# Kernel optimization log

Hardware: AMD Instinct MI355X
Metric: run time of the kernel (lower is better)

Reference implementation:

```python
import jax, jax.numpy as jnp
from jax import lax
import numpy as np

# StyleLayer config (see init_kwargs)
B, CIN, COUT, SDIM, K, H, W = 8, 512, 512, 512, 3, 64, 64
UP, DOWN = 2, 2
PAD = (9, 8, 9, 8)            # px0, px1, py0, py1 (computed in __init__)
GAIN = 2.0 ** 0.5             # non-rgb gain
SLOPE = 0.2                   # non-rgb negative slope
CLAMP = 256.0                 # conv_clamp
TAPS = 12                     # filter_size * factor
TMP_SRATE = 128.0             # max(sr_in, sr_out) * lrelu_sampling
CUTOFF = 32.0
WIDTH = 32.0                  # half_width * 2


def _kaiser_lowpass(numtaps, cutoff, width, fs):
    """Equivalent of scipy.signal.firwin(numtaps, cutoff, width=width, fs=fs)."""
    nyq = fs / 2.0
    atten = 2.285 * (numtaps - 1) * np.pi * (width / nyq) + 7.95  # kaiser_atten
    if atten > 50:
        beta = 0.1102 * (atten - 8.7)
    elif atten > 21:
        beta = 0.5842 * (atten - 21) ** 0.4 + 0.07886 * (atten - 21)
    else:
        beta = 0.0
    m = np.arange(numtaps) - (numtaps - 1) / 2.0
    fc = cutoff / nyq
    h = fc * np.sinc(fc * m) * np.kaiser(numtaps, beta)
    h /= h.sum()
    return jnp.asarray(h, jnp.float32)


def _upfirdn2d_sep(x, f, up, down, padding, gain):
    """upfirdn2d reference with separable 1D filter (flip_filter=False)."""
    Bx, C, Hx, Wx = x.shape
    px0, px1, py0, py1 = padding
    if up > 1:  # zero insertion
        x = x.reshape(Bx, C, Hx, 1, Wx, 1)
        x = jnp.pad(x, [(0, 0), (0, 0), (0, 0), (0, up - 1), (0, 0), (0, up - 1)])
        x = x.reshape(Bx, C, Hx * up, Wx * up)
    x = jnp.pad(x, [(0, 0), (0, 0), (py0, py1), (px0, px1)])
    fk = (f * (gain ** 0.5))[::-1].astype(x.dtype)  # gain**(ndim/2) per pass, flipped
    t = fk.shape[0]
    dn = ('NCHW', 'OIHW', 'NCHW')
    kx = jnp.tile(fk.reshape(1, 1, 1, t), (C, 1, 1, 1))
    x = lax.conv_general_dilated(x, kx, (1, 1), [(0, 0), (0, 0)], dimension_numbers=dn, feature_group_count=C)
    ky = jnp.tile(fk.reshape(1, 1, t, 1), (C, 1, 1, 1))
    x = lax.conv_general_dilated(x, ky, (1, 1), [(0, 0), (0, 0)], dimension_numbers=dn, feature_group_count=C)
    if down > 1:
        x = x[:, :, ::down, ::down]
    return x


def setup_inputs() -> dict:
    key = jax.random.key(0)
    ks = jax.random.split(key, 4)
    f = _kaiser_lowpass(TAPS, CUTOFF, WIDTH, TMP_SRATE)
    return {
        'x': jax.random.normal(ks[0], (B, CIN, H, W), jnp.float32),
        'w': jax.random.normal(ks[1], (B, SDIM), jnp.float32),
        'affine_weight': jax.random.normal(ks[2], (CIN, SDIM), jnp.float32),
        'affine_bias': jnp.ones((CIN,), jnp.float32),  # bias.data.fill_(1.0)
        'conv_weight': jax.random.normal(ks[3], (COUT, CIN, K, K), jnp.float32),
        'bias': jnp.zeros((COUT,), jnp.float32),
        'up_filter': f,
        'down_filter': f,
        'ema': jnp.ones((1,), jnp.float32),
    }


def reference(x, w, affine_weight, affine_bias, conv_weight, bias, up_filter, down_filter, ema):
    input_gain = lax.rsqrt(ema[0])
    # affine: Linear with scale = 1/sqrt(style_dim), linear activation
    s = w @ (affine_weight * (1.0 / SDIM ** 0.5)).T + affine_bias            # [B, CIN]
    # modulated conv weight construction
    wt = conv_weight[None] * s[:, None, :, None, None] * (1.0 / (CIN * K * K) ** 0.5)
    d = lax.rsqrt(jnp.sum(jnp.square(wt), axis=(2, 3, 4)) + 1e-8)            # demod
    wt = wt * d[:, :, None, None, None] * input_gain
    # grouped conv: one group per sample, padding = kernel_size - 1
    xg = x.reshape(1, B * CIN, H, W)
    wg = wt.reshape(B * COUT, CIN, K, K)
    y = lax.conv_general_dilated(xg, wg, (1, 1), [(K - 1, K - 1), (K - 1, K - 1)],
                                 dimension_numbers=('NCHW', 'OIHW', 'NCHW'),
                                 feature_group_count=B)
    y = y.reshape(B, COUT, H + K - 1, W + K - 1)
    # filtered_lrelu reference: bias -> up-FIR (gain=up^2) -> lrelu*gain, clamp -> FIR-down
    y = y + bias[None, :, None, None]
    y = _upfirdn2d_sep(y, up_filter, UP, 1, PAD, float(UP * UP))
    y = jnp.clip(jnp.where(y >= 0, y, y * SLOPE) * GAIN, -CLAMP, CLAMP)
    y = _upfirdn2d_sep(y, down_filter, 1, DOWN, (0, 0, 0, 0), 1.0)
    return y
```

## Files before the change

### kernel.cpp

```cpp
#include <hip/hip_runtime.h>
#include <hip/hip_bf16.h>


#define B_    8
#define CIN_  512
#define COUT_ 512
#define SDIM_ 512
#define H_    64
#define W_    64
#define HO_   66
#define NPIX  4356
#define XP    68

typedef short s8v  __attribute__((ext_vector_type(8)));
typedef float f4v  __attribute__((ext_vector_type(4)));

#define WAITV3() asm volatile("s_waitcnt vmcnt(3)" ::: "memory")
#define WAITV0() asm volatile("s_waitcnt vmcnt(0)" ::: "memory")

__global__ __launch_bounds__(256) void k_style_s(
    const float* __restrict__ w, const float* __restrict__ aw,
    const float* __restrict__ ab, float* __restrict__ s) {
    const int t  = blockIdx.x * 4 + (threadIdx.x >> 6);
    const int ln = threadIdx.x & 63;
    const int b = t >> 9, c = t & 511;
    const float* wp = w + b * SDIM_;
    const float* ap = aw + (size_t)c * SDIM_;
    float acc = 0.f;
    #pragma unroll
    for (int j = 0; j < 8; ++j) { int k = ln + 64 * j; acc += wp[k] * ap[k]; }
    #pragma unroll
    for (int off = 32; off; off >>= 1) acc += __shfl_down(acc, off, 64);
    if (ln == 0) s[t] = acc * 0.044194173824159216f + ab[c];
}

__global__ __launch_bounds__(256) void k_style_coef(
    const float* __restrict__ s, const float* __restrict__ r,
    const float* __restrict__ ema, float* __restrict__ coef) {
    const int t  = blockIdx.x * 4 + (threadIdx.x >> 6);
    const int ln = threadIdx.x & 63;
    const int b = t >> 9, o = t & 511;
    const float* sp = s + b * 512;
    const float* rp = r + (size_t)o * 512;
    float acc = 0.f;
    #pragma unroll
    for (int j = 0; j < 8; ++j) {
        int k = ln + 64 * j;
        float sv = sp[k];
        acc += sv * sv * rp[k];
    }
    #pragma unroll
    for (int off = 32; off; off >>= 1) acc += __shfl_down(acc, off, 64);
    if (ln == 0) {
        float d  = rsqrtf(acc * (1.0f / 4608.0f) + 1e-8f);
        coef[t] = d * rsqrtf(ema[0]) * 0.014731391274719739f;
    }
}

__global__ __launch_bounds__(256) void k_prep_w(const float* __restrict__ cw,
                                                __hip_bfloat16* __restrict__ wb,
                                                float* __restrict__ r) {
    __shared__ float sm[2304];
    const int base = blockIdx.x * 256;
    const int tid  = threadIdx.x;
    const float* src = cw + (size_t)base * 9;
    for (int i = tid; i < 2304; i += 256) sm[i] = src[i];
    __syncthreads();
    float a = 0.f;
    ushort u[9];
    #pragma unroll
    for (int k = 0; k < 9; ++k) {
        float v = sm[tid * 9 + k];
        a += v * v;
        __hip_bfloat16 h = __float2bfloat16(v);
        u[k] = *reinterpret_cast<ushort*>(&h);
    }
    r[base + tid] = a;
    ushort* wbu = reinterpret_cast<ushort*>(wb);
    #pragma unroll
    for (int tap = 0; tap < 9; ++tap)
        wbu[tap * 262144 + base + tid] = u[tap];
}

__global__ __launch_bounds__(256) void k_prep_x(const float* __restrict__ x,
                                                const float* __restrict__ s,
                                                __hip_bfloat16* __restrict__ xt) {
    __shared__ float tile[64][65];
    const int y = blockIdx.x;
    const int b = blockIdx.y;
    const int tid = threadIdx.x;
    const bool yin = (y >= 2 && y < 66);
    __hip_bfloat16* orow = xt + ((size_t)(b * XP + y)) * XP * 512;
    for (int c0 = 0; c0 < 512; c0 += 64) {
        if (yin) {
            for (int i = tid; i < 64 * 64; i += 256) {
                int c = i >> 6, xx = i & 63;
                tile[c][xx] = x[(((size_t)b * 512 + c0 + c) * 64 + (y - 2)) * 64 + xx]
                              * s[b * 512 + c0 + c];
            }
        }
        __syncthreads();
        for (int j = tid; j < 68 * 8; j += 256) {
            int xx = j >> 3, cg = j & 7;
            bool xin = yin && (xx >= 2 && xx < 66);
            union { ushort u[8]; float4 f4; } pk;
            #pragma unroll
            for (int k = 0; k < 8; ++k) {
                float v = xin ? tile[cg * 8 + k][xx - 2] : 0.f;
                __hip_bfloat16 h = __float2bfloat16(v);
                pk.u[k] = *reinterpret_cast<ushort*>(&h);
            }
            *reinterpret_cast<float4*>(orow + (size_t)xx * 512 + c0 + cg * 8) = pk.f4;
        }
        __syncthreads();
    }
}

__device__ __forceinline__ void gload16u(const char* base, unsigned voff, void* l) {
    __builtin_amdgcn_global_load_lds(
        (const __attribute__((address_space(1))) unsigned*)(base + voff),
        (__attribute__((address_space(3))) unsigned*)l, 16, 0, 0);
}

__global__ __launch_bounds__(512) void k_conv_mfma(
    const __hip_bfloat16* __restrict__ wb, const __hip_bfloat16* __restrict__ xt,
    const float* __restrict__ coef, const float* __restrict__ bias,
    __hip_bfloat16* __restrict__ y1)
{
    __shared__ __hip_bfloat16 lds[3][12288];

    const int bid   = blockIdx.x;
    const int dbl   = bid < 48;
    const int rr2   = dbl ? bid : bid - 48;
    const int xcd   = rr2 & 7;
    const int j     = dbl ? (rr2 >> 3) : (6 + (rr2 >> 3));
    const int ntile = dbl ? 2 : 1;

    const int tid = threadIdx.x, wv = tid >> 6, ln = tid & 63;
    const int wm = wv >> 1, wn = wv & 1;

    const int srow = tid >> 2, ssl = tid & 3;
    const unsigned swzs = (unsigned)((ssl ^ ((srow >> 1) & 3)) << 3);
    int aoff[4], boff[4];
    #pragma unroll
    for (int f = 0; f < 4; ++f) {
        int r  = wm * 64 + f * 16 + (ln & 15);
        aoff[f] = (r * 32 + (((ln >> 4) ^ ((r >> 1) & 3)) << 3)) * 2;
        int rb = wn * 64 + f * 16 + (ln & 15);
        boff[f] = (8192 + rb * 32 + (((ln >> 4) ^ ((rb >> 1) & 3)) << 3)) * 2;
    }
    const char* wbB = (const char*)wb;

    for (int tt = 0; tt < ntile; ++tt) {
        const int pos  = (tt == 0) ? j : (64 + j);
        const int flat = xcd * 70 + pos;
        const int pi = flat % 35;
        const int t2 = flat / 35;
        const int b  = t2 & 7;
        const int o0 = (t2 >> 3) * 256;
        const int p0 = pi * 128;

        const char* xtB = (const char*)(xt + (size_t)b * XP * XP * 512);
        unsigned voffA0 = ((unsigned)(o0 + srow) * 512u + swzs) * 2u;
        unsigned voffA1 = ((unsigned)(o0 + 128 + srow) * 512u + swzs) * 2u;
        unsigned voffB0;
        {
            int p = p0 + srow; if (p > NPIX - 1) p = NPIX - 1;
            int py = (int)(((unsigned)p * 63551u) >> 22);
            int px = p - py * 66;
            voffB0 = ((unsigned)(py * XP + px) * 512u + swzs) * 2u;
        }

        f4v acc[4][4];
        #pragma unroll
        for (int fm = 0; fm < 4; ++fm)
            #pragma unroll
            for (int fn = 0; fn < 4; ++fn) acc[fm][fn] = (f4v){0.f, 0.f, 0.f, 0.f};

        auto stage = [&](int st, int buf) {
            int tap = st >> 4;
            int ki  = (tap * 11) >> 5;
            int kj  = tap - ki * 3;
            unsigned ccb  = (unsigned)(st & 15) << 6;
            unsigned offA = (unsigned)tap * 524288u + ccb;
            unsigned offB = (unsigned)(ki * XP + kj) * 1024u + ccb;
            __hip_bfloat16* dst = &lds[buf][0] + wv * 512;
            gload16u(wbB, voffA0 + offA, dst);
            gload16u(wbB, voffA1 + offA, dst + 4096);
            gload16u(xtB, voffB0 + offB, dst + 8192);
        };

        auto compute = [&](int buf) {
            const char* base = (const char*)&lds[buf][0];
            s8v af[4], bfv[4];
            #pragma unroll
            for (int f = 0; f < 4; ++f) {
                af[f]  = *reinterpret_cast<const s8v*>(base + aoff[f]);
                bfv[f] = *reinterpret_cast<const s8v*>(base + boff[f]);
            }
            #pragma unroll
            for (int fm = 0; fm < 4; ++fm)
                #pragma unroll
                for (int fn = 0; fn < 4; ++fn)
                    acc[fm][fn] = __builtin_amdgcn_mfma_f32_16x16x32_bf16(
                        af[fm], bfv[fn], acc[fm][fn], 0, 0, 0);
        };

        stage(0, 0);
        stage(1, 1);

        #pragma unroll 1
        for (int st = 0; st < 141; st += 3) {
            WAITV3(); __builtin_amdgcn_s_barrier();
            compute(0); stage(st + 2, 2);
            WAITV3(); __builtin_amdgcn_s_barrier();
            compute(1); stage(st + 3, 0);
            WAITV3(); __builtin_amdgcn_s_barrier();
            compute(2); stage(st + 4, 1);
        }
        WAITV3(); __builtin_amdgcn_s_barrier();
        compute(0); stage(143, 2);
        WAITV3(); __builtin_amdgcn_s_barrier();
        compute(1);
        WAITV0(); __builtin_amdgcn_s_barrier();
        compute(2);

        #pragma unroll
        for (int fm = 0; fm < 4; ++fm) {
            #pragma unroll
            for (int fn = 0; fn < 4; ++fn) {
                int p = p0 + wn * 64 + fn * 16 + (ln & 15);
                if (p < NPIX) {
                    int ob = o0 + wm * 64 + fm * 16 + (ln >> 4) * 4;
                    #pragma unroll
                    for (int jj = 0; jj < 4; ++jj) {
                        int o = ob + jj;
                        float v = acc[fm][fn][jj] * coef[b * 512 + o] + bias[o];
                        y1[((size_t)(b * 512 + o)) * NPIX + p] = __float2bfloat16(v);
                    }
                }
            }
        }
    }
}

__global__ __launch_bounds__(256) void k_style_fir(
    const __hip_bfloat16* __restrict__ y1, const float* __restrict__ uf,
    const float* __restrict__ df, float* __restrict__ out)
{
    __shared__ float smA[5632];
    __shared__ float smB[3200];
    float* It = smA;
    float* hu = smB;
    float* zt = smA;
    float* dh = smB;

    const int img = blockIdx.z;
    const int oy0 = blockIdx.y * 32;
    const int ox0 = blockIdx.x * 32;
    const int tid = threadIdx.x;
    const __hip_bfloat16* I = y1 + (size_t)img * NPIX;

    float cu[12], cd[12];
    #pragma unroll
    for (int q = 0; q < 12; ++q) { cu[q] = uf[q]; cd[q] = df[q]; }

    const int ty = tid >> 5, tx = tid & 31;
    const int ty4 = tid >> 4, tx4 = tid & 15;

    #pragma unroll
    for (int k = 0; k < 6; ++k) {
        int rr = ty + 8 * k; if (rr >= 42) break;
        int gy = oy0 - 4 + rr;
        bool yin = (gy >= 0 && gy < HO_);
        #pragma unroll
        for (int j = 0; j < 2; ++j) {
            int cc = tx + 32 * j; if (cc >= 42) continue;
            int gx = ox0 - 4 + cc;
            float v = 0.f;
            if (yin && gx >= 0 && gx < HO_) v = __bfloat162float(I[gy * HO_ + gx]);
            It[rr * 44 + cc] = v;
        }
    }
    __syncthreads();

    #pragma unroll
    for (int k = 0; k < 6; ++k) {
        int m = ty + 8 * k; if (m >= 42) break;
        #pragma unroll
        for (int j = 0; j < 2; ++j) {
            int h = tx + 32 * j; if (h >= 37) continue;
            float v[6];
            #pragma unroll
            for (int q = 0; q < 6; ++q) v[q] = It[m * 44 + h + 5 - q];
            float e = 0.f, o = 0.f;
            #pragma unroll
            for (int q = 0; q < 6; ++q) { e += cu[2 * q] * v[q]; o += cu[2 * q + 1] * v[q]; }
            *reinterpret_cast<float2*>(hu + m * 76 + 2 * h) = make_float2(2.f * e, 2.f * o);
        }
    }
    __syncthreads();

    {
        int rx  = tid % 74;
        int seg = tid / 74;
        if (seg < 3) {
            int r0  = seg * 13;
            int cnt = (seg == 2) ? 11 : 13;
            float wnd[6];
            #pragma unroll
            for (int i = 0; i < 5; ++i) wnd[i] = hu[(r0 + i) * 76 + rx];
            #pragma unroll
            for (int i = 0; i < 13; ++i) {
                if (i < cnt) {
                    wnd[5] = hu[(r0 + i + 5) * 76 + rx];
                    float e = 0.f, o = 0.f;
                    #pragma unroll
                    for (int q = 0; q < 6; ++q) {
                        e += cu[2 * q] * wnd[5 - q];
                        o += cu[2 * q + 1] * wnd[5 - q];
                    }
                    e *= 2.f; o *= 2.f;
                    e = (e >= 0.f ? e : e * 0.2f) * 1.4142135623730951f;
                    o = (o >= 0.f ? o : o * 0.2f) * 1.4142135623730951f;
                    e = fminf(fmaxf(e, -256.f), 256.f);
                    o = fminf(fmaxf(o, -256.f), 256.f);
                    int r = r0 + i;
                    zt[(2 * r) * 76 + rx]     = e;
                    zt[(2 * r + 1) * 76 + rx] = o;
                    #pragma unroll
                    for (int k2 = 0; k2 < 5; ++k2) wnd[k2] = wnd[k2 + 1];
                }
            }
        }
    }
    __syncthreads();

    #pragma unroll
    for (int k = 0; k < 5; ++k) {
        int ry = ty4 + 16 * k; if (ry >= 74) break;
        const float* zr = zt + ry * 76 + 4 * tx4;
        float z[14];
        #pragma unroll
        for (int t = 0; t < 7; ++t) {
            float2 p2 = *reinterpret_cast<const float2*>(zr + 2 * t);
            z[2 * t] = p2.x; z[2 * t + 1] = p2.y;
        }
        float a0 = 0.f, a1 = 0.f;
        #pragma unroll
        for (int u = 0; u < 12; ++u) { a0 += z[u] * cd[11 - u]; a1 += z[u + 2] * cd[11 - u]; }
        *reinterpret_cast<float2*>(dh + ry * 36 + 2 * tx4) = make_float2(a0, a1);
    }
    __syncthreads();

    #pragma unroll
    for (int k = 0; k < 2; ++k) {
        int r2 = ty + 8 * k;
        float d[14];
        #pragma unroll
        for (int v = 0; v < 14; ++v) d[v] = dh[(4 * r2 + v) * 36 + tx];
        float a0 = 0.f, a1 = 0.f;
        #pragma unroll
        for (int v = 0; v < 12; ++v) { a0 += d[v] * cd[11 - v]; a1 += d[v + 2] * cd[11 - v]; }
        float* op = out + (size_t)img * 64 * 64 + (oy0 + 2 * r2) * 64 + ox0 + tx;
        op[0]  = a0;
        op[64] = a1;
    }
}

extern "C" void kernel_launch(void* const* d_in, const int* in_sizes, int n_in,
                              void* d_out, int out_size, void* d_ws, size_t ws_size,
                              hipStream_t stream) {
    const float* x    = (const float*)d_in[0];
    const float* w    = (const float*)d_in[1];
    const float* aw   = (const float*)d_in[2];
    const float* ab   = (const float*)d_in[3];
    const float* cw   = (const float*)d_in[4];
    const float* bias = (const float*)d_in[5];
    const float* uf   = (const float*)d_in[6];
    const float* df   = (const float*)d_in[7];
    const float* ema  = (const float*)d_in[8];
    float* out = (float*)d_out;

    float* ws   = (float*)d_ws;
    float* s_   = ws;
    float* coef = ws + 4096;
    float* r_   = ws + 8192;
    __hip_bfloat16* y1 = (__hip_bfloat16*)(ws + 270336);
    __hip_bfloat16* xt = (__hip_bfloat16*)(ws + 270336 + 8921088);
    __hip_bfloat16* wb = (__hip_bfloat16*)(ws + 270336 + 8921088 + 9469952);

    k_style_s   <<<1024, 256, 0, stream>>>(w, aw, ab, s_);
    k_prep_w    <<<1024, 256, 0, stream>>>(cw, wb, r_);
    k_style_coef<<<1024, 256, 0, stream>>>(s_, r_, ema, coef);
    k_prep_x    <<<dim3(68, 8), 256, 0, stream>>>(x, s_, xt);
    k_conv_mfma <<<512, 512, 0, stream>>>(wb, xt, coef, bias, y1);
    k_style_fir <<<dim3(2, 2, 4096), 256, 0, stream>>>(y1, uf, df, out);
}
```

Measured before the change: 361.3 us.

## Widen conv pixel tile to 160 and drop the double-tile block scheduling

Changes the implicit-GEMM conv tile from 256x128 to 256x160 output pixels, giving 448 blocks that each handle exactly one tile instead of the previous mix of one- and two-tile blocks. The last tile overlaps the previous one to avoid bounds checks, and two extra waves load the additional B rows with an adjusted vmcnt wait. The aim is better load balance across the 256 CUs and more MFMA work per staged A tile, at the cost of more accumulator registers, larger LDS buffers, and some redundant computation in the overlapping tile.

```diff
diff --git a/kernel.cpp b/kernel.cpp
--- a/kernel.cpp
+++ b/kernel.cpp
@@ -15,6 +15,7 @@
 typedef short s8v  __attribute__((ext_vector_type(8)));
 typedef float f4v  __attribute__((ext_vector_type(4)));
 
+#define WAITV4() asm volatile("s_waitcnt vmcnt(4)" ::: "memory")
 #define WAITV3() asm volatile("s_waitcnt vmcnt(3)" ::: "memory")
 #define WAITV0() asm volatile("s_waitcnt vmcnt(0)" ::: "memory")
 
@@ -122,123 +123,131 @@
         (__attribute__((address_space(3))) unsigned*)l, 16, 0, 0);
 }
 
-__global__ __launch_bounds__(512) void k_conv_mfma(
+__global__ __launch_bounds__(512, 4) void k_conv_mfma(
     const __hip_bfloat16* __restrict__ wb, const __hip_bfloat16* __restrict__ xt,
     const float* __restrict__ coef, const float* __restrict__ bias,
     __hip_bfloat16* __restrict__ y1)
 {
-    __shared__ __hip_bfloat16 lds[3][12288];
-
-    const int bid   = blockIdx.x;
-    const int dbl   = bid < 48;
-    const int rr2   = dbl ? bid : bid - 48;
-    const int xcd   = rr2 & 7;
-    const int j     = dbl ? (rr2 >> 3) : (6 + (rr2 >> 3));
-    const int ntile = dbl ? 2 : 1;
+    __shared__ __hip_bfloat16 lds[3][13312];
+
+    const int bid  = blockIdx.x;
+    const int flat = (bid & 7) * 56 + (bid >> 3);
+    const int pi = flat % 28;
+    const int t2 = flat / 28;
+    const int b  = t2 & 7;
+    const int o0 = (t2 >> 3) * 256;
+    const int p0 = (pi < 27) ? pi * 160 : (NPIX - 160);
 
     const int tid = threadIdx.x, wv = tid >> 6, ln = tid & 63;
     const int wm = wv >> 1, wn = wv & 1;
 
+    const char* wbB = (const char*)wb;
+    const char* xtB = (const char*)(xt + (size_t)b * XP * XP * 512);
     const int srow = tid >> 2, ssl = tid & 3;
     const unsigned swzs = (unsigned)((ssl ^ ((srow >> 1) & 3)) << 3);
-    int aoff[4], boff[4];
+    unsigned voffA0 = ((unsigned)(o0 + srow) * 512u + swzs) * 2u;
+    unsigned voffA1 = ((unsigned)(o0 + 128 + srow) * 512u + swzs) * 2u;
+    unsigned voffB0, voffB1 = 0;
+    {
+        int p = p0 + srow;
+        int py = (int)(((unsigned)p * 63551u) >> 22);
+        int px = p - py * 66;
+        voffB0 = ((unsigned)(py * XP + px) * 512u + swzs) * 2u;
+    }
+    if (wv < 2) {
+        int j2 = 512 + tid;
+        int row2 = j2 >> 2, sl2 = j2 & 3;
+        unsigned swz2 = (unsigned)((sl2 ^ ((row2 >> 1) & 3)) << 3);
+        int p = p0 + row2;
+        int py = (int)(((unsigned)p * 63551u) >> 22);
+        int px = p - py * 66;
+        voffB1 = ((unsigned)(py * XP + px) * 512u + swz2) * 2u;
+    }
+
+    int aoff[4], boff[5];
     #pragma unroll
     for (int f = 0; f < 4; ++f) {
         int r  = wm * 64 + f * 16 + (ln & 15);
         aoff[f] = (r * 32 + (((ln >> 4) ^ ((r >> 1) & 3)) << 3)) * 2;
-        int rb = wn * 64 + f * 16 + (ln & 15);
+    }
+    #pragma unroll
+    for (int f = 0; f < 5; ++f) {
+        int rb = wn * 80 + f * 16 + (ln & 15);
         boff[f] = (8192 + rb * 32 + (((ln >> 4) ^ ((rb >> 1) & 3)) << 3)) * 2;
     }
-    const char* wbB = (const char*)wb;
-
-    for (int tt = 0; tt < ntile; ++tt) {
-        const int pos  = (tt == 0) ? j : (64 + j);
-        const int flat = xcd * 70 + pos;
-        const int pi = flat % 35;
-        const int t2 = flat / 35;
-        const int b  = t2 & 7;
-        const int o0 = (t2 >> 3) * 256;
-        const int p0 = pi * 128;
-
-        const char* xtB = (const char*)(xt + (size_t)b * XP * XP * 512);
-        unsigned voffA0 = ((unsigned)(o0 + srow) * 512u + swzs) * 2u;
-        unsigned voffA1 = ((unsigned)(o0 + 128 + srow) * 512u + swzs) * 2u;
-        unsigned voffB0;
-        {
-            int p = p0 + srow; if (p > NPIX - 1) p = NPIX - 1;
-            int py = (int)(((unsigned)p * 63551u) >> 22);
-            int px = p - py * 66;
-            voffB0 = ((unsigned)(py * XP + px) * 512u + swzs) * 2u;
-        }
-
-        f4v acc[4][4];
-        #pragma unroll
-        for (int fm = 0; fm < 4; ++fm)
-            #pragma unroll
-            for (int fn = 0; fn < 4; ++fn) acc[fm][fn] = (f4v){0.f, 0.f, 0.f, 0.f};
-
-        auto stage = [&](int st, int buf) {
-            int tap = st >> 4;
-            int ki  = (tap * 11) >> 5;
-            int kj  = tap - ki * 3;
-            unsigned ccb  = (unsigned)(st & 15) << 6;
-            unsigned offA = (unsigned)tap * 524288u + ccb;
-            unsigned offB = (unsigned)(ki * XP + kj) * 1024u + ccb;
-            __hip_bfloat16* dst = &lds[buf][0] + wv * 512;
-            gload16u(wbB, voffA0 + offA, dst);
-            gload16u(wbB, voffA1 + offA, dst + 4096);
-            gload16u(xtB, voffB0 + offB, dst + 8192);
-        };
-
-        auto compute = [&](int buf) {
-            const char* base = (const char*)&lds[buf][0];
-            s8v af[4], bfv[4];
-            #pragma unroll
-            for (int f = 0; f < 4; ++f) {
-                af[f]  = *reinterpret_cast<const s8v*>(base + aoff[f]);
-                bfv[f] = *reinterpret_cast<const s8v*>(base + boff[f]);
-            }
+
+    f4v acc[4][5];
+    #pragma unroll
+    for (int fm = 0; fm < 4; ++fm)
+        #pragma unroll
+        for (int fn = 0; fn < 5; ++fn) acc[fm][fn] = (f4v){0.f, 0.f, 0.f, 0.f};
+
+    auto stage = [&](int st, int buf) {
+        int tap = st >> 4;
+        int ki  = (tap * 11) >> 5;
+        int kj  = tap - ki * 3;
+        unsigned ccb  = (unsigned)(st & 15) << 6;
+        unsigned offA = (unsigned)tap * 524288u + ccb;
+        unsigned offB = (unsigned)(ki * XP + kj) * 1024u + ccb;
+        __hip_bfloat16* dst = &lds[buf][0] + wv * 512;
+        gload16u(wbB, voffA0 + offA, dst);
+        gload16u(wbB, voffA1 + offA, dst + 4096);
+        gload16u(xtB, voffB0 + offB, dst + 8192);
+        if (wv < 2)
+            gload16u(xtB, voffB1 + offB, dst + 12288);
+    };
+
+    auto compute = [&](int buf) {
+        const char* base = (const char*)&lds[buf][0];
+        s8v af[4];
+        #pragma unroll
+        for (int f = 0; f < 4; ++f)
+            af[f] = *reinterpret_cast<const s8v*>(base + aoff[f]);
+        #pragma unroll
+        for (int fn = 0; fn < 5; ++fn) {
+            s8v bv = *reinterpret_cast<const s8v*>(base + boff[fn]);
             #pragma unroll
             for (int fm = 0; fm < 4; ++fm)
-                #pragma unroll
-                for (int fn = 0; fn < 4; ++fn)
-                    acc[fm][fn] = __builtin_amdgcn_mfma_f32_16x16x32_bf16(
-                        af[fm], bfv[fn], acc[fm][fn], 0, 0, 0);
-        };
-
-        stage(0, 0);
-        stage(1, 1);
-
-        #pragma unroll 1
-        for (int st = 0; st < 141; st += 3) {
-            WAITV3(); __builtin_amdgcn_s_barrier();
-            compute(0); stage(st + 2, 2);
-            WAITV3(); __builtin_amdgcn_s_barrier();
-            compute(1); stage(st + 3, 0);
-            WAITV3(); __builtin_amdgcn_s_barrier();
-            compute(2); stage(st + 4, 1);
-        }
-        WAITV3(); __builtin_amdgcn_s_barrier();
-        compute(0); stage(143, 2);
-        WAITV3(); __builtin_amdgcn_s_barrier();
-        compute(1);
-        WAITV0(); __builtin_amdgcn_s_barrier();
-        compute(2);
-
-        #pragma unroll
-        for (int fm = 0; fm < 4; ++fm) {
-            #pragma unroll
-            for (int fn = 0; fn < 4; ++fn) {
-                int p = p0 + wn * 64 + fn * 16 + (ln & 15);
-                if (p < NPIX) {
-                    int ob = o0 + wm * 64 + fm * 16 + (ln >> 4) * 4;
-                    #pragma unroll
-                    for (int jj = 0; jj < 4; ++jj) {
-                        int o = ob + jj;
-                        float v = acc[fm][fn][jj] * coef[b * 512 + o] + bias[o];
-                        y1[((size_t)(b * 512 + o)) * NPIX + p] = __float2bfloat16(v);
-                    }
-                }
+                acc[fm][fn] = __builtin_amdgcn_mfma_f32_16x16x32_bf16(
+                    af[fm], bv, acc[fm][fn], 0, 0, 0);
+        }
+    };
+
+    stage(0, 0);
+    stage(1, 1);
+
+    #pragma unroll 1
+    for (int st = 0; st < 141; st += 3) {
+        if (wv < 2) { WAITV4(); } else { WAITV3(); }
+        __builtin_amdgcn_s_barrier();
+        compute(0); stage(st + 2, 2);
+        if (wv < 2) { WAITV4(); } else { WAITV3(); }
+        __builtin_amdgcn_s_barrier();
+        compute(1); stage(st + 3, 0);
+        if (wv < 2) { WAITV4(); } else { WAITV3(); }
+        __builtin_amdgcn_s_barrier();
+        compute(2); stage(st + 4, 1);
+    }
+    if (wv < 2) { WAITV4(); } else { WAITV3(); }
+    __builtin_amdgcn_s_barrier();
+    compute(0); stage(143, 2);
+    if (wv < 2) { WAITV4(); } else { WAITV3(); }
+    __builtin_amdgcn_s_barrier();
+    compute(1);
+    WAITV0(); __builtin_amdgcn_s_barrier();
+    compute(2);
+
+    #pragma unroll
+    for (int fm = 0; fm < 4; ++fm) {
+        #pragma unroll
+        for (int fn = 0; fn < 5; ++fn) {
+            int p = p0 + wn * 80 + fn * 16 + (ln & 15);
+            int ob = o0 + wm * 64 + fm * 16 + (ln >> 4) * 4;
+            #pragma unroll
+            for (int jj = 0; jj < 4; ++jj) {
+                int o = ob + jj;
+                float v = acc[fm][fn][jj] * coef[b * 512 + o] + bias[o];
+                y1[((size_t)(b * 512 + o)) * NPIX + p] = __float2bfloat16(v);
             }
         }
     }
@@ -394,6 +403,6 @@
     k_prep_w    <<<1024, 256, 0, stream>>>(cw, wb, r_);
     k_style_coef<<<1024, 256, 0, stream>>>(s_, r_, ema, coef);
     k_prep_x    <<<dim3(68, 8), 256, 0, stream>>>(x, s_, xt);
-    k_conv_mfma <<<512, 512, 0, stream>>>(wb, xt, coef, bias, y1);
+    k_conv_mfma <<<448, 512, 0, stream>>>(wb, xt, coef, bias, y1);
     k_style_fir <<<dim3(2, 2, 4096), 256, 0, stream>>>(y1, uf, df, out);
 }
```

New measurement: 395.9 us. 9.6% more time.
